# Performance work log

Hardware: AMD Instinct MI355X
Metric: run time of the kernel (lower is better)

Reference implementation:

```python
import jax, jax.numpy as jnp
import numpy as np

DIM, DEPTH, HEADS = 1024, 6, 16
B, N = 2, 1024
QB = 128.0   # 8-bit activation absmax quant: Qb = 2**(8-1)
EPS = 1e-5


def setup_inputs() -> dict:
    key = jax.random.key(0)
    ks = jax.random.split(key, 4)
    x = jax.random.normal(ks[0], (B, N, DIM), dtype=jnp.float32)
    # BitLinear weights (per layer, two per FFN block), latent fp weights
    ff_w1 = jax.random.normal(ks[1], (DEPTH, DIM, DIM), dtype=jnp.float32) * 0.02
    ff_w2 = jax.random.normal(ks[2], (DEPTH, DIM, DIM), dtype=jnp.float32) * 0.02
    # LayerNorm params (inside FeedForward) and final norm
    ff_ln_g = jnp.ones((DEPTH, DIM), jnp.float32)
    ff_ln_b = jnp.zeros((DEPTH, DIM), jnp.float32)
    final_ln_g = jnp.ones((DIM,), jnp.float32)
    final_ln_b = jnp.zeros((DIM,), jnp.float32)
    return dict(x=x, ff_ln_g=ff_ln_g, ff_ln_b=ff_ln_b, ff_w1=ff_w1,
                ff_w2=ff_w2, final_ln_g=final_ln_g, final_ln_b=final_ln_b)


def layernorm(x, g, b):
    m = jnp.mean(x, axis=-1, keepdims=True)
    v = jnp.mean((x - m) ** 2, axis=-1, keepdims=True)
    return (x - m) * jax.lax.rsqrt(v + EPS) * g + b


def bitlinear(x, w):
    # BitNet b1: binarize weights around their mean, absmax-quantize activations to 8 bits,
    # int-style matmul, then rescale by beta*gamma/Qb.
    alpha = jnp.mean(w)
    w_b = jnp.sign(w - alpha)                 # ternary/binary weights {-1,0,+1}
    beta = jnp.mean(jnp.abs(w))               # ||W||_1 / (n*m)
    gamma = jnp.max(jnp.abs(x))               # activation absmax
    x_q = jnp.clip(x * (QB / gamma), -QB + EPS, QB - EPS)
    y = jnp.einsum('...i,oi->...o', x_q, w_b)
    return y * (beta * gamma / QB)


def attend(x):
    # non-flash multi-head self-attention, q=k=v=x (Attend has no projections)
    b, n, d = x.shape
    dh = d // HEADS
    q = x.reshape(b, n, HEADS, dh).transpose(0, 2, 1, 3)          # bhnd
    scores = jnp.einsum('bhid,bhjd->bhij', q, q) * (dh ** -0.5)   # [B,H,N,N]
    attn = jax.nn.softmax(scores, axis=-1)
    out = jnp.einsum('bhij,bhjd->bhid', attn, q)
    return out.transpose(0, 2, 1, 3).reshape(b, n, d)


def reference(x, ff_ln_g, ff_ln_b, ff_w1, ff_w2, final_ln_g, final_ln_b):
    for i in range(DEPTH):
        x = attend(x) + x
        h = layernorm(x, ff_ln_g[i], ff_ln_b[i])
        h = bitlinear(h, ff_w1[i])
        h = jax.nn.gelu(h, approximate=False)   # torch nn.GELU default = exact
        h = bitlinear(h, ff_w2[i])
        x = h + x
    return layernorm(x, final_ln_g, final_ln_b)
```

## Files before the change

### kernel.cpp

```cpp
#include <hip/hip_runtime.h>
#include <math.h>

typedef __attribute__((ext_vector_type(4))) float f32x4;
typedef __attribute__((ext_vector_type(8))) _Float16 f16x8;

__device__ __forceinline__ f32x4 mfma16h(f16x8 a, f16x8 b, f32x4 c){
  return __builtin_amdgcn_mfma_f32_16x16x32_f16(a, b, c, 0, 0, 0);
}
__device__ __forceinline__ void gload_lds16(const void* g, void* l){
  __builtin_amdgcn_global_load_lds((const __attribute__((address_space(1))) void*)g,
                                   (__attribute__((address_space(3))) void*)l, 16, 0, 0);
}

#define EXPC 0.1803368801111204f

__global__ __launch_bounds__(256) void k_wstats(const float* __restrict__ w1, const float* __restrict__ w2,
                                                double* __restrict__ dsum, double* __restrict__ dabs){
  const int mat = blockIdx.y;
  const float* wp = (mat < 6) ? (w1 + (size_t)mat*1048576) : (w2 + (size_t)(mat-6)*1048576);
  const f32x4* wv = (const f32x4*)wp + (size_t)blockIdx.x*8192;
  double s = 0.0, a = 0.0;
  for (int j = 0; j < 32; j++){
    f32x4 v = wv[j*256 + threadIdx.x];
    s += (double)v.x + (double)v.y + (double)v.z + (double)v.w;
    a += (double)fabsf(v.x) + (double)fabsf(v.y) + (double)fabsf(v.z) + (double)fabsf(v.w);
  }
  for (int d = 1; d < 64; d <<= 1){ s += __shfl_xor(s, d); a += __shfl_xor(a, d); }
  __shared__ double red[8];
  const int w = threadIdx.x >> 6;
  if ((threadIdx.x & 63) == 0){ red[w*2] = s; red[w*2+1] = a; }
  __syncthreads();
  if (threadIdx.x == 0){
    double S = red[0]+red[2]+red[4]+red[6], A = red[1]+red[3]+red[5]+red[7];
    atomicAdd(&dsum[mat], S);
    atomicAdd(&dabs[mat], A);
  }
}

__global__ __launch_bounds__(256) void k_binarize(const float* __restrict__ w1, const float* __restrict__ w2,
                                                  const double* __restrict__ dsum, _Float16* __restrict__ wb){
  const int blk = blockIdx.x;
  const int mat = blk >> 9;
  const float alpha = (float)(dsum[mat] * (1.0/1048576.0));
  const float* wp = (mat < 6) ? (w1 + (size_t)mat*1048576) : (w2 + (size_t)(mat-6)*1048576);
  const size_t off = (size_t)(blk & 511)*2048 + (size_t)threadIdx.x*8;
  const int n = (int)(off >> 10), k = (int)(off & 1023);
  f32x4 v0 = *(const f32x4*)(wp + off), v1 = *(const f32x4*)(wp + off + 4);
  float vv[8] = {v0.x,v0.y,v0.z,v0.w,v1.x,v1.y,v1.z,v1.w};
  f16x8 pk;
  #pragma unroll
  for (int e = 0; e < 8; e++){
    float d = vv[e] - alpha;
    pk[e] = d > 0.f ? (_Float16)1.0f : (d < 0.f ? (_Float16)(-1.0f) : (_Float16)0.0f);
  }
  const size_t addr = (size_t)mat*1048576 + (size_t)n*1024 + (size_t)((k & ~63) + ((k & 63) ^ ((n&7)*8)));
  *(f16x8*)&wb[addr] = pk;
}

__global__ __launch_bounds__(256) void k_presplit(const float* __restrict__ x,
                                                  _Float16* __restrict__ Kh, _Float16* __restrict__ Kl,
                                                  _Float16* __restrict__ Vh, _Float16* __restrict__ Vl){
  __shared__ _Float16 lh[64*72], ll[64*72];
  const int t = blockIdx.x, bh = blockIdx.y, b = bh>>4, h = bh&15;
  const int n = threadIdx.x>>2, c0 = (threadIdx.x&3)*16;
  const float* src = x + (size_t)b*1048576 + (size_t)(t*64+n)*1024 + h*64 + c0;
  const size_t kbase = ((size_t)bh*1024 + t*64 + n)*64;
  const int sw = ((((n>>4)&1)<<2) | (((n>>3)&1)<<1) | (n&1)) * 8;
  #pragma unroll
  for (int j = 0; j < 2; j++){
    f32x4 v0 = *(const f32x4*)(src + j*8);
    f32x4 v1 = *(const f32x4*)(src + j*8 + 4);
    float vv[8] = {v0.x,v0.y,v0.z,v0.w,v1.x,v1.y,v1.z,v1.w};
    f16x8 Hv, Lv;
    #pragma unroll
    for (int e = 0; e < 8; e++){
      _Float16 hh = (_Float16)vv[e];
      Hv[e] = hh; Lv[e] = (_Float16)(vv[e] - (float)hh);
      const int d = c0 + j*8 + e;
      lh[d*72 + n] = Hv[e]; ll[d*72 + n] = Lv[e];
    }
    const int db = c0 + j*8;
    *(f16x8*)&Kh[kbase + (db ^ sw)] = Hv;
    *(f16x8*)&Kl[kbase + (db ^ sw)] = Lv;
  }
  __syncthreads();
  const int d = threadIdx.x>>2, n0c = (threadIdx.x&3)*16;
  const size_t vbase = ((size_t)bh*64 + d)*1024 + t*64;
  const int sw2 = (d&7)*8;
  #pragma unroll
  for (int j = 0; j < 2; j++){
    f16x8 Hv, Lv;
    #pragma unroll
    for (int e = 0; e < 8; e++){
      Hv[e] = lh[d*72 + n0c + j*8 + e];
      Lv[e] = ll[d*72 + n0c + j*8 + e];
    }
    const int nb = n0c + j*8;
    *(f16x8*)&Vh[vbase + (nb ^ sw2)] = Hv;
    *(f16x8*)&Vl[vbase + (nb ^ sw2)] = Lv;
  }
}

__global__ __launch_bounds__(256) void k_attn(const _Float16* __restrict__ Kh, const _Float16* __restrict__ Kl,
                                              const _Float16* __restrict__ Vh, const _Float16* __restrict__ Vl,
                                              const float* __restrict__ xin, float* __restrict__ xout){
  __shared__ _Float16 smb[40960];
  _Float16* qs_h = smb + 32768;
  _Float16* qs_l = smb + 36864;
  const int tid = threadIdx.x, w = tid>>6, l = tid&63, g = l>>4, r16 = l&15;
  const int bh = blockIdx.x, qt = blockIdx.y, b = bh>>4, h = bh&15;
  const _Float16* Kbh = Kh + (size_t)bh*65536;
  const _Float16* Kbl = Kl + (size_t)bh*65536;

  size_t koffK[2], voff[2];
  int cbj[2];
  #pragma unroll
  for (int j = 0; j < 2; j++){
    const int cb = (j*4 + w)*64, c = cb + l;
    const int p  = c>>3;
    const int kp = (p&32) | ((p&12)<<1) | ((p&16)>>2) | (p&3);
    cbj[j]   = cb;
    koffK[j] = (size_t)kp*64 + (size_t)(l&7)*8;
    voff[j]  = ((size_t)bh*64 + (c>>3))*1024 + (size_t)(c&7)*8;
  }
  #define ASTAGE(buf, t) { _Float16* Bp = smb + (buf)*16384;                         \
    _Pragma("unroll")                                                                 \
    for (int j = 0; j < 2; j++){                                                      \
      gload_lds16(Kbh + (size_t)(t)*4096 + koffK[j], Bp + cbj[j]*8);                  \
      gload_lds16(Kbl + (size_t)(t)*4096 + koffK[j], Bp + 4096 + cbj[j]*8);           \
      gload_lds16(Vh + voff[j] + (t)*64, Bp + 8192 + cbj[j]*8);                       \
      gload_lds16(Vl + voff[j] + (t)*64, Bp + 12288 + cbj[j]*8);                      \
    } }

  const _Float16* Qsh = Kbh + (size_t)qt*4096;
  const _Float16* Qsl = Kbl + (size_t)qt*4096;
  #pragma unroll
  for (int j = 0; j < 2; j++){
    const int cb = cbj[j];
    gload_lds16(Qsh + (size_t)(cb + l)*8, qs_h + cb*8);
    gload_lds16(Qsl + (size_t)(cb + l)*8, qs_l + cb*8);
  }
  ASTAGE(0, 0);
  __syncthreads();
  const int qrow = w*16 + r16;
  const int phq8 = (((w&1)<<2) | (((r16>>3)&1)<<1) | (r16&1)) * 8;
  const int swk8 = ((((r16>>3)&1)<<2) | (((r16>>2)&1)<<1) | (r16&1)) * 8;
  const int swr8 = (r16&7)*8;
  const f16x8 aqh0 = *(const f16x8*)&qs_h[qrow*64 + ((g*8) ^ phq8)];
  const f16x8 aqh1 = *(const f16x8*)&qs_h[qrow*64 + ((32 + g*8) ^ phq8)];
  const f16x8 aql0 = *(const f16x8*)&qs_l[qrow*64 + ((g*8) ^ phq8)];
  const f16x8 aql1 = *(const f16x8*)&qs_l[qrow*64 + ((32 + g*8) ^ phq8)];
  float mI = -1e30f, lI = 0.f;
  f32x4 acc[4];
  #pragma unroll
  for (int i = 0; i < 4; i++) acc[i] = (f32x4){0.f,0.f,0.f,0.f};

  for (int t = 0; t < 16; t++){
    if (t < 15) ASTAGE((t+1)&1, t+1);
    const _Float16* kt_h = smb + (t&1)*16384;
    const _Float16* kt_l = kt_h + 4096;
    const _Float16* vt_h = kt_h + 8192;
    const _Float16* vt_l = kt_h + 12288;
    f32x4 s[4];
    #pragma unroll
    for (int c = 0; c < 4; c++){
      const int rk = c*16 + r16;
      const f16x8 kh0 = *(const f16x8*)&kt_h[rk*64 + ((g*8) ^ swk8)];
      const f16x8 kh1 = *(const f16x8*)&kt_h[rk*64 + ((32+g*8) ^ swk8)];
      const f16x8 kl0 = *(const f16x8*)&kt_l[rk*64 + ((g*8) ^ swk8)];
      const f16x8 kl1 = *(const f16x8*)&kt_l[rk*64 + ((32+g*8) ^ swk8)];
      f32x4 z = (f32x4){0.f,0.f,0.f,0.f};
      z = mfma16h(kh0, aqh0, z);
      z = mfma16h(kh1, aqh1, z);
      z = mfma16h(kh0, aql0, z);
      z = mfma16h(kh1, aql1, z);
      z = mfma16h(kl0, aqh0, z);
      z = mfma16h(kl1, aqh1, z);
      s[c] = z;
    }
    float rmax = s[0][0];
    #pragma unroll
    for (int c = 0; c < 4; c++)
      #pragma unroll
      for (int i = 0; i < 4; i++) rmax = fmaxf(rmax, s[c][i]);
    rmax = fmaxf(rmax, __shfl_xor(rmax, 16));
    rmax = fmaxf(rmax, __shfl_xor(rmax, 32));
    if (__any(rmax - mI > 44.36f)){
      const float mn = fmaxf(mI, rmax);
      const float fac = exp2f((mI - mn)*EXPC);
      lI *= fac;
      mI = mn;
      #pragma unroll
      for (int i = 0; i < 4; i++){
        const float fi = __shfl(fac, g*4 + i);
        #pragma unroll
        for (int dc = 0; dc < 4; dc++) acc[dc][i] *= fi;
      }
    }
    const float mC = mI*EXPC;
    float rsum = 0.f;
    f16x8 aph[2], apl[2];
    #pragma unroll
    for (int c = 0; c < 4; c++)
      #pragma unroll
      for (int i = 0; i < 4; i++){
        const float p = exp2f(fmaf(s[c][i], EXPC, -mC));
        const _Float16 ph = (_Float16)p;
        aph[c>>1][(c&1)*4 + i] = ph;
        apl[c>>1][(c&1)*4 + i] = (_Float16)(p - (float)ph);
        rsum += p;
      }
    rsum += __shfl_xor(rsum, 16);
    rsum += __shfl_xor(rsum, 32);
    lI += rsum;
    #pragma unroll
    for (int ks = 0; ks < 2; ks++){
      #pragma unroll
      for (int dc = 0; dc < 4; dc++){
        const int vr = dc*16 + r16;
        const f16x8 bvh = *(const f16x8*)&vt_h[vr*64 + ((ks*32 + g*8) ^ swr8)];
        const f16x8 bvl = *(const f16x8*)&vt_l[vr*64 + ((ks*32 + g*8) ^ swr8)];
        acc[dc] = mfma16h(aph[ks], bvh, acc[dc]);
        acc[dc] = mfma16h(apl[ks], bvh, acc[dc]);
        acc[dc] = mfma16h(aph[ks], bvl, acc[dc]);
      }
    }
    __syncthreads();
  }
  #undef ASTAGE
  #pragma unroll
  for (int i = 0; i < 4; i++){
    const float li = __shfl(lI, g*4 + i);
    const float inv = 1.f/li;
    const int row = qt*64 + w*16 + g*4 + i;
    #pragma unroll
    for (int dc = 0; dc < 4; dc++){
      const size_t idx = (size_t)b*1048576 + (size_t)row*1024 + h*64 + dc*16 + r16;
      xout[idx] = acc[dc][i]*inv + xin[idx];
    }
  }
}

template<int SPLIT>
__global__ __launch_bounds__(256) void k_ln(const float* __restrict__ x, const float* __restrict__ gg,
                                            const float* __restrict__ bb, float* __restrict__ outf,
                                            _Float16* __restrict__ Oh, _Float16* __restrict__ Ol){
  const int row = blockIdx.x*4 + (threadIdx.x>>6);
  const int lane = threadIdx.x & 63;
  const float* xr = x + (size_t)row*1024;
  f32x4 v[4];
  float s = 0.f, q = 0.f;
  #pragma unroll
  for (int c = 0; c < 2; c++){
    v[c*2]   = *(const f32x4*)(xr + c*512 + lane*8);
    v[c*2+1] = *(const f32x4*)(xr + c*512 + lane*8 + 4);
    #pragma unroll
    for (int e = 0; e < 4; e++){
      s += v[c*2][e] + v[c*2+1][e];
      q += v[c*2][e]*v[c*2][e] + v[c*2+1][e]*v[c*2+1][e];
    }
  }
  for (int d = 1; d < 64; d <<= 1){ s += __shfl_xor(s,d); q += __shfl_xor(q,d); }
  const float mean = s * (1.f/1024.f);
  const float var  = q * (1.f/1024.f) - mean*mean;
  const float rstd = rsqrtf(var + 1e-5f);
  #pragma unroll
  for (int c = 0; c < 2; c++){
    const int col = c*512 + lane*8;
    f32x4 g0 = *(const f32x4*)(gg + col), g1 = *(const f32x4*)(gg + col + 4);
    f32x4 b0 = *(const f32x4*)(bb + col), b1 = *(const f32x4*)(bb + col + 4);
    float h[8];
    #pragma unroll
    for (int e = 0; e < 4; e++){
      h[e]   = (v[c*2][e]  -mean)*rstd*g0[e] + b0[e];
      h[e+4] = (v[c*2+1][e]-mean)*rstd*g1[e] + b1[e];
    }
    if (SPLIT){
      f16x8 Hv, Lv;
      #pragma unroll
      for (int e = 0; e < 8; e++){
        _Float16 hh = (_Float16)h[e];
        Hv[e] = hh; Lv[e] = (_Float16)(h[e] - (float)hh);
      }
      const size_t addr = (size_t)row*1024 + c*512 + (lane>>3)*64 + (((lane&7)*8) ^ ((row&7)*8));
      *(f16x8*)&Oh[addr] = Hv;
      *(f16x8*)&Ol[addr] = Lv;
    } else {
      f32x4 o0, o1;
      #pragma unroll
      for (int e = 0; e < 4; e++){ o0[e] = h[e]; o1[e] = h[e+4]; }
      *(f32x4*)(outf + (size_t)row*1024 + col) = o0;
      *(f32x4*)(outf + (size_t)row*1024 + col + 4) = o1;
    }
  }
}

template<int MODE>
__global__ __launch_bounds__(256) void k_gemm(const _Float16* __restrict__ Ah, const _Float16* __restrict__ Al,
                                              const _Float16* __restrict__ Wg,
                                              float* __restrict__ out32,
                                              _Float16* __restrict__ Oh, _Float16* __restrict__ Ol,
                                              const double* __restrict__ dabs_slot){
  __shared__ _Float16 smb[24576];
  const int tid = threadIdx.x, w = tid>>6, l = tid&63, g = l>>4, r16 = l&15;
  const int wm = w>>1, wn = w&1;
  const int n0 = blockIdx.x*64, m0 = blockIdx.y*64;
  const float scale = (float)(*dabs_slot * (1.0/1048576.0));
  const int swr = (r16&7)*8;
  f32x4 acc[2][2] = {};
  #define STAGE(buf, k0) { _Float16* Bp = smb + (buf)*12288;                              \
    _Pragma("unroll")                                                                     \
    for (int j = 0; j < 2; j++){                                                          \
      const int cb = (j*4 + w)*64; const int c = cb + l;                                  \
      const int r = c>>3; const int cc = (c&7)*8;                                         \
      gload_lds16(Ah + (size_t)(m0 + r)*1024 + (k0) + cc, Bp + cb*8);                     \
      gload_lds16(Al + (size_t)(m0 + r)*1024 + (k0) + cc, Bp + 4096 + cb*8);              \
      gload_lds16(Wg + (size_t)(n0 + r)*1024 + (k0) + cc, Bp + 8192 + cb*8);              \
    } }
  STAGE(0, 0);
  __syncthreads();
  for (int t = 0; t < 16; t++){
    if (t < 15) STAGE((t+1)&1, (t+1)*64);
    const _Float16* Bp = smb + (t&1)*12288;
    #pragma unroll
    for (int kk = 0; kk < 2; kk++){
      f16x8 ah[2], al[2], bf[2];
      const int col = (kk*32 + g*8) ^ swr;
      #pragma unroll
      for (int mi = 0; mi < 2; mi++){
        const int row = wm*32 + mi*16 + r16;
        ah[mi] = *(const f16x8*)&Bp[row*64 + col];
        al[mi] = *(const f16x8*)&Bp[4096 + row*64 + col];
      }
      #pragma unroll
      for (int ni = 0; ni < 2; ni++){
        const int row = wn*32 + ni*16 + r16;
        bf[ni] = *(const f16x8*)&Bp[8192 + row*64 + col];
      }
      #pragma unroll
      for (int mi = 0; mi < 2; mi++)
        #pragma unroll
        for (int ni = 0; ni < 2; ni++){
          acc[mi][ni] = mfma16h(ah[mi], bf[ni], acc[mi][ni]);
          acc[mi][ni] = mfma16h(al[mi], bf[ni], acc[mi][ni]);
        }
    }
    __syncthreads();
  }
  #undef STAGE
  #pragma unroll
  for (int mi = 0; mi < 2; mi++)
    #pragma unroll
    for (int ni = 0; ni < 2; ni++)
      #pragma unroll
      for (int i = 0; i < 4; i++){
        const int rr = m0 + wm*32 + mi*16 + g*4 + i;
        const int cc = n0 + wn*32 + ni*16 + r16;
        float vv = acc[mi][ni][i] * scale;
        if (MODE == 0){
          vv = 0.5f*vv*(1.f + erff(vv*0.70710678118f));
          _Float16 hh = (_Float16)vv;
          const size_t addr = (size_t)rr*1024 + (cc & ~63) + ((cc & 63) ^ ((rr&7)*8));
          Oh[addr] = hh;
          Ol[addr] = (_Float16)(vv - (float)hh);
        } else {
          out32[(size_t)rr*1024 + cc] += vv;
        }
      }
}

extern "C" void kernel_launch(void* const* d_in, const int* in_sizes, int n_in,
                              void* d_out, int out_size, void* d_ws, size_t ws_size,
                              hipStream_t stream){
  const float* x_in = (const float*)d_in[0];
  const float* ln_g = (const float*)d_in[1];
  const float* ln_b = (const float*)d_in[2];
  const float* w1   = (const float*)d_in[3];
  const float* w2   = (const float*)d_in[4];
  const float* fg   = (const float*)d_in[5];
  const float* fb   = (const float*)d_in[6];

  char* ws = (char*)d_ws;
  double*   dsum  = (double*)ws;
  double*   dabs  = (double*)(ws + 96);
  _Float16* wb = (_Float16*)(ws + 256);
  size_t o = 256 + 12ull*1048576ull*2ull;
  float* xA = (float*)(ws + o); o += 2048ull*1024*4;
  float* xB = (float*)(ws + o); o += 2048ull*1024*4;
  _Float16* Kh = (_Float16*)(ws + o); o += 2048ull*1024*2;
  _Float16* Kl = (_Float16*)(ws + o); o += 2048ull*1024*2;
  _Float16* Vh = (_Float16*)(ws + o); o += 2048ull*1024*2;
  _Float16* Vl = (_Float16*)(ws + o); o += 2048ull*1024*2;
  _Float16* Ahb = (_Float16*)(ws + o); o += 2048ull*1024*2;
  _Float16* Alb = (_Float16*)(ws + o); o += 2048ull*1024*2;
  _Float16* Ghb = (_Float16*)(ws + o); o += 2048ull*1024*2;
  _Float16* Glb = (_Float16*)(ws + o); o += 2048ull*1024*2;

  hipMemsetAsync(ws, 0, 256, stream);
  k_wstats  <<<dim3(32,12), 256, 0, stream>>>(w1, w2, dsum, dabs);
  k_binarize<<<6144,        256, 0, stream>>>(w1, w2, dsum, wb);

  const float* xc = x_in;
  for (int i = 0; i < 6; i++){
    float* xn = (i & 1) ? xB : xA;
    k_presplit<<<dim3(16,32), 256, 0, stream>>>(xc, Kh, Kl, Vh, Vl);
    k_attn    <<<dim3(32,16), 256, 0, stream>>>(Kh, Kl, Vh, Vl, xc, xn);
    k_ln<1>   <<<512, 256, 0, stream>>>(xn, ln_g + (size_t)i*1024, ln_b + (size_t)i*1024,
                                        nullptr, Ahb, Alb);
    k_gemm<0> <<<dim3(16,32), 256, 0, stream>>>(Ahb, Alb, wb + (size_t)i*1048576,
                                                nullptr, Ghb, Glb, &dabs[i]);
    k_gemm<1> <<<dim3(16,32), 256, 0, stream>>>(Ghb, Glb, wb + (size_t)(6+i)*1048576,
                                                xn, nullptr, nullptr, &dabs[6+i]);
    xc = xn;
  }
  k_ln<0><<<512, 256, 0, stream>>>(xc, fg, fb, (float*)d_out, nullptr, nullptr);
}
```

Measured before the change: 520.4 us.

## Fuse K/V fp16 split and layout into second FFN GEMM epilogue

```diff
diff --git a/kernel.cpp b/kernel.cpp
--- a/kernel.cpp
+++ b/kernel.cpp
@@ -13,6 +13,7 @@
 }
 
 #define EXPC 0.1803368801111204f
+#define PHI(n) (((((n)>>3)&1)<<2) | ((((n)>>1)&1)<<1) | ((n)&1))
 
 __global__ __launch_bounds__(256) void k_wstats(const float* __restrict__ w1, const float* __restrict__ w2,
                                                 double* __restrict__ dsum, double* __restrict__ dabs){
@@ -65,7 +66,7 @@
   const int n = threadIdx.x>>2, c0 = (threadIdx.x&3)*16;
   const float* src = x + (size_t)b*1048576 + (size_t)(t*64+n)*1024 + h*64 + c0;
   const size_t kbase = ((size_t)bh*1024 + t*64 + n)*64;
-  const int sw = ((((n>>4)&1)<<2) | (((n>>3)&1)<<1) | (n&1)) * 8;
+  const int sw = PHI(n)*8;
   #pragma unroll
   for (int j = 0; j < 2; j++){
     f32x4 v0 = *(const f32x4*)(src + j*8);
@@ -89,15 +90,9 @@
   const int sw2 = (d&7)*8;
   #pragma unroll
   for (int j = 0; j < 2; j++){
-    f16x8 Hv, Lv;
-    #pragma unroll
-    for (int e = 0; e < 8; e++){
-      Hv[e] = lh[d*72 + n0c + j*8 + e];
-      Lv[e] = ll[d*72 + n0c + j*8 + e];
-    }
     const int nb = n0c + j*8;
-    *(f16x8*)&Vh[vbase + (nb ^ sw2)] = Hv;
-    *(f16x8*)&Vl[vbase + (nb ^ sw2)] = Lv;
+    *(f16x8*)&Vh[vbase + (nb ^ sw2)] = *(const f16x8*)&lh[d*72 + nb];
+    *(f16x8*)&Vl[vbase + (nb ^ sw2)] = *(const f16x8*)&ll[d*72 + nb];
   }
 }
 
@@ -143,8 +138,8 @@
   ASTAGE(0, 0);
   __syncthreads();
   const int qrow = w*16 + r16;
-  const int phq8 = (((w&1)<<2) | (((r16>>3)&1)<<1) | (r16&1)) * 8;
-  const int swk8 = ((((r16>>3)&1)<<2) | (((r16>>2)&1)<<1) | (r16&1)) * 8;
+  const int phq8 = PHI(qrow)*8;
+  const int swk8 = (r16&7)*8;
   const int swr8 = (r16&7)*8;
   const f16x8 aqh0 = *(const f16x8*)&qs_h[qrow*64 + ((g*8) ^ phq8)];
   const f16x8 aqh1 = *(const f16x8*)&qs_h[qrow*64 + ((32 + g*8) ^ phq8)];
@@ -300,7 +295,9 @@
                                               const _Float16* __restrict__ Wg,
                                               float* __restrict__ out32,
                                               _Float16* __restrict__ Oh, _Float16* __restrict__ Ol,
-                                              const double* __restrict__ dabs_slot){
+                                              const double* __restrict__ dabs_slot,
+                                              _Float16* __restrict__ Kh, _Float16* __restrict__ Kl,
+                                              _Float16* __restrict__ Vh, _Float16* __restrict__ Vl){
   __shared__ _Float16 smb[24576];
   const int tid = threadIdx.x, w = tid>>6, l = tid&63, g = l>>4, r16 = l&15;
   const int wm = w>>1, wn = w&1;
@@ -348,6 +345,10 @@
     __syncthreads();
   }
   #undef STAGE
+  _Float16* kh_t = smb;
+  _Float16* kl_t = smb + 4608;
+  _Float16* lhv  = smb + 9216;
+  _Float16* llv  = smb + 13824;
   #pragma unroll
   for (int mi = 0; mi < 2; mi++)
     #pragma unroll
@@ -364,9 +365,37 @@
           Oh[addr] = hh;
           Ol[addr] = (_Float16)(vv - (float)hh);
         } else {
-          out32[(size_t)rr*1024 + cc] += vv;
+          const size_t idx = (size_t)rr*1024 + cc;
+          const float xnew = out32[idx] + vv;
+          out32[idx] = xnew;
+          if (Kh){
+            const int nl = wm*32 + mi*16 + g*4 + i;
+            const int dl = wn*32 + ni*16 + r16;
+            const _Float16 hh = (_Float16)xnew;
+            const _Float16 lo = (_Float16)(xnew - (float)hh);
+            kh_t[nl*72 + dl] = hh;  kl_t[nl*72 + dl] = lo;
+            lhv [dl*72 + nl] = hh;  llv [dl*72 + nl] = lo;
+          }
         }
       }
+  if (MODE == 1 && Kh){
+    __syncthreads();
+    const int n = tid>>2, c0q = (tid&3)*16;
+    const int bh = (blockIdx.y>>4)*16 + blockIdx.x;
+    const int tseq = blockIdx.y & 15;
+    const size_t kbase = ((size_t)bh*1024 + tseq*64 + n)*64;
+    const int swn = PHI(n)*8;
+    const size_t vbase = ((size_t)bh*64 + n)*1024 + tseq*64;
+    const int sw2 = (n&7)*8;
+    #pragma unroll
+    for (int j = 0; j < 2; j++){
+      const int db = c0q + j*8;
+      *(f16x8*)&Kh[kbase + (db ^ swn)] = *(const f16x8*)&kh_t[n*72 + db];
+      *(f16x8*)&Kl[kbase + (db ^ swn)] = *(const f16x8*)&kl_t[n*72 + db];
+      *(f16x8*)&Vh[vbase + (db ^ sw2)] = *(const f16x8*)&lhv[n*72 + db];
+      *(f16x8*)&Vl[vbase + (db ^ sw2)] = *(const f16x8*)&llv[n*72 + db];
+    }
+  }
 }
 
 extern "C" void kernel_launch(void* const* d_in, const int* in_sizes, int n_in,
@@ -399,18 +428,22 @@
   hipMemsetAsync(ws, 0, 256, stream);
   k_wstats  <<<dim3(32,12), 256, 0, stream>>>(w1, w2, dsum, dabs);
   k_binarize<<<6144,        256, 0, stream>>>(w1, w2, dsum, wb);
+  k_presplit<<<dim3(16,32), 256, 0, stream>>>(x_in, Kh, Kl, Vh, Vl);
 
   const float* xc = x_in;
   for (int i = 0; i < 6; i++){
     float* xn = (i & 1) ? xB : xA;
-    k_presplit<<<dim3(16,32), 256, 0, stream>>>(xc, Kh, Kl, Vh, Vl);
+    const bool last = (i == 5);
     k_attn    <<<dim3(32,16), 256, 0, stream>>>(Kh, Kl, Vh, Vl, xc, xn);
     k_ln<1>   <<<512, 256, 0, stream>>>(xn, ln_g + (size_t)i*1024, ln_b + (size_t)i*1024,
                                         nullptr, Ahb, Alb);
     k_gemm<0> <<<dim3(16,32), 256, 0, stream>>>(Ahb, Alb, wb + (size_t)i*1048576,
-                                                nullptr, Ghb, Glb, &dabs[i]);
+                                                nullptr, Ghb, Glb, &dabs[i],
+                                                nullptr, nullptr, nullptr, nullptr);
     k_gemm<1> <<<dim3(16,32), 256, 0, stream>>>(Ghb, Glb, wb + (size_t)(6+i)*1048576,
-                                                xn, nullptr, nullptr, &dabs[6+i]);
+                                                xn, nullptr, nullptr, &dabs[6+i],
+                                                last ? nullptr : Kh, last ? nullptr : Kl,
+                                                last ? nullptr : Vh, last ? nullptr : Vl);
     xc = xn;
   }
   k_ln<0><<<512, 256, 0, stream>>>(xc, fg, fb, (float*)d_out, nullptr, nullptr);
```

Result: no change. 512.8 us (-1.5%).
